# Optimization experiments

Measured on AMD Instinct MI355X. Metric: run time of the kernel, lower is better.

Reference implementation:

```python
import jax, jax.numpy as jnp
import numpy as np


def _mlp(x, w1, b1, w2, b2):
    # Linear->ReLU->Linear->ReLU (torch Linear: y = x @ W.T + b)
    return jax.nn.relu(jax.nn.relu(x @ w1.T + b1) @ w2.T + b2)


def _lstm_cell(x, h, c, wih, whh, bih, bhh):
    g = x @ wih.T + bih + h @ whh.T + bhh
    i, f, gg, o = jnp.split(g, 4, axis=-1)  # torch gate order i,f,g,o
    c = jax.nn.sigmoid(f) * c + jax.nn.sigmoid(i) * jnp.tanh(gg)
    h = jax.nn.sigmoid(o) * jnp.tanh(c)
    return h, c


def _decode(iml, img_features, mlp1_w1, mlp1_b1, mlp1_w2, mlp1_b2,
            mlp2_w1, mlp2_b1, mlp2_w2, mlp2_b2,
            lstm_wih, lstm_whh, lstm_bih, lstm_bhh,
            attn_w, attn_b, fc_w, fc_b, emb, max_seq_len):
    # iml: [B, H, K] flattened conv map; annotations are channel vectors per position
    ann = jnp.transpose(iml, (0, 2, 1))          # [B, K, H]
    mean_ann = jnp.mean(iml, axis=-1)            # [B, H]
    h0 = _mlp(mean_ann, mlp1_w1, mlp1_b1, mlp1_w2, mlp1_b2)
    c0 = _mlp(mean_ann, mlp2_w1, mlp2_b1, mlp2_w2, mlp2_b2)
    H = h0.shape[-1]
    # attn = Linear(2H, 1) on cat(ann, h): decompose into two dot products.
    w_a, w_h = attn_w[:H], attn_w[H:]
    e_ann = ann @ w_a + attn_b[0]                # [B, K], annotation part precomputed

    def step(carry, _):
        x, h, c = carry
        h, c = _lstm_cell(x, h, c, lstm_wih, lstm_whh, lstm_bih, lstm_bhh)
        e = e_ann + (h @ w_h)[:, None]           # [B, K] fused concat+linear scores
        alpha = jax.nn.softmax(e, axis=-1)       # [B, K]
        cs = jnp.einsum('bk,bkh->bh', alpha, ann)  # weighted context [B, H]
        logits = jnp.concatenate([h, cs], axis=-1) @ fc_w.T + fc_b  # [B, V]
        sample = jnp.argmax(logits, axis=-1)     # greedy token
        return (emb[sample], h, c), (logits, sample)

    _, (logits, samples) = jax.lax.scan(step, (img_features, h0, c0), None, length=max_seq_len)
    # scan stacks on axis 0 (time); move to [B, T, ...]
    return jnp.transpose(logits, (1, 0, 2)), jnp.transpose(samples, (1, 0))


def setup_inputs() -> dict:
    B, K, H, E, V, T = 64, 196, 512, 512, 10000, 30
    key = jax.random.key(0)
    ks = jax.random.split(key, 11)
    inv = 1.0 / np.sqrt(H)
    r = lambda i, shape, scale=1.0: jax.random.normal(ks[i], shape, jnp.float32) * scale
    return {
        'iml': r(0, (B, H, K)),
        'img_features': r(1, (B, E)),
        'mlp1_w1': r(2, (H, H), inv), 'mlp1_b1': jnp.zeros(H, jnp.float32),
        'mlp1_w2': r(3, (H, H), inv), 'mlp1_b2': jnp.zeros(H, jnp.float32),
        'mlp2_w1': r(4, (H, H), inv), 'mlp2_b1': jnp.zeros(H, jnp.float32),
        'mlp2_w2': r(5, (H, H), inv), 'mlp2_b2': jnp.zeros(H, jnp.float32),
        'lstm_wih': r(6, (4 * H, E), inv), 'lstm_whh': r(7, (4 * H, H), inv),
        'lstm_bih': jnp.zeros(4 * H, jnp.float32), 'lstm_bhh': jnp.zeros(4 * H, jnp.float32),
        'attn_w': r(8, (2 * H,), inv), 'attn_b': jnp.zeros(1, jnp.float32),
        'fc_w': r(9, (V, 2 * H), inv), 'fc_b': jnp.zeros(V, jnp.float32),
        'emb': r(10, (V, E)),
        'max_seq_len': T,
    }


def reference(iml, img_features, mlp1_w1, mlp1_b1, mlp1_w2, mlp1_b2,
              mlp2_w1, mlp2_b1, mlp2_w2, mlp2_b2,
              lstm_wih, lstm_whh, lstm_bih, lstm_bhh,
              attn_w, attn_b, fc_w, fc_b, emb, max_seq_len):
    all_logits, sampled_ids = _decode(
        iml, img_features, mlp1_w1, mlp1_b1, mlp1_w2, mlp1_b2,
        mlp2_w1, mlp2_b1, mlp2_w2, mlp2_b2,
        lstm_wih, lstm_whh, lstm_bih, lstm_bhh,
        attn_w, attn_b, fc_w, fc_b, emb, max_seq_len)
    return all_logits, sampled_ids
```

## Files before the change

### kernel.cpp

```cpp
#include <hip/hip_runtime.h>
#include <hip/hip_bf16.h>

#define B 64
#define KDIM 196
#define H 512
#define V 10000
#define TSTEPS 30
#define VP 10240
#define NVC 40
#define NSLOT 8
#define SLOTSTRIDE 16

typedef unsigned long long u64;
typedef unsigned int u32;

__device__ __forceinline__ u64 pack_vi(float v, int idx) {
    u32 kb = __float_as_uint(v);
    kb = (kb & 0x80000000u) ? ~kb : (kb | 0x80000000u);
    return ((u64)kb << 32) | (u32)(~(u32)idx);
}
__device__ __forceinline__ u32 best_idx_of_slots(const u64* __restrict__ slots, int b) {
    u64 best = slots[b * SLOTSTRIDE];
#pragma unroll
    for (int s = 1; s < NSLOT; ++s) { u64 v = slots[b * SLOTSTRIDE + s]; if (v > best) best = v; }
    return ~(u32)best;
}


__global__ void k_transpose_fc(const float* __restrict__ fcw, float* __restrict__ dst, int coloff) {
    __shared__ float tile[32][33];
    int v0 = blockIdx.x * 32, i0 = blockIdx.y * 32;
    int tx = threadIdx.x, ty = threadIdx.y;
#pragma unroll
    for (int r = 0; r < 32; r += 8) {
        int v = v0 + ty + r; int i = i0 + tx;
        tile[ty + r][tx] = (v < V) ? fcw[(size_t)v * 1024 + coloff + i] : 0.f;
    }
    __syncthreads();
#pragma unroll
    for (int r = 0; r < 32; r += 8) {
        int i = i0 + ty + r; int v = v0 + tx;
        dst[(size_t)i * VP + v] = tile[tx][ty + r];
    }
}

__global__ void k_build_wct(const float* __restrict__ wih, const float* __restrict__ whh,
                            float* __restrict__ dst) {
    __shared__ float tile[32][33];
    int j0 = blockIdx.x * 32, i0 = blockIdx.y * 32;
    int tx = threadIdx.x, ty = threadIdx.y;
#pragma unroll
    for (int r = 0; r < 32; r += 8) {
        int j = j0 + ty + r; int i = i0 + tx;
        tile[ty + r][tx] = (i < 512) ? wih[(size_t)j * 512 + i] : whh[(size_t)j * 512 + i - 512];
    }
    __syncthreads();
#pragma unroll
    for (int r = 0; r < 32; r += 8) {
        int i = i0 + ty + r; int j = j0 + tx;
        dst[(size_t)i * 2048 + j] = tile[tx][ty + r];
    }
}

__global__ void k_mean(const float* __restrict__ iml, float* __restrict__ mean) {
    int w = threadIdx.x >> 6, lane = threadIdx.x & 63;
    int row = blockIdx.x * 4 + w;
    const float* p = iml + (size_t)row * KDIM;
    float s = p[lane] + p[lane + 64] + p[lane + 128] + ((lane < 4) ? p[lane + 192] : 0.f);
#pragma unroll
    for (int off = 32; off; off >>= 1) s += __shfl_down(s, off);
    if (lane == 0) mean[row] = s * (1.f / 196.f);
}

__global__ void k_e_alpha(const float* __restrict__ iml, const float* __restrict__ attn_w,
                          float* __restrict__ alpha) {
    int b = blockIdx.x, t = threadIdx.x;
    __shared__ float wa[512];
    wa[t] = attn_w[t]; wa[t + 256] = attn_w[t + 256];
    __syncthreads();
    float acc = 0.f;
    if (t < KDIM) {
        const float* p = iml + (size_t)b * 512 * KDIM + t;
#pragma unroll 8
        for (int h = 0; h < 512; ++h) acc += p[(size_t)h * KDIM] * wa[h];
    }
    __shared__ float red[256];
    red[t] = (t < KDIM) ? acc : -__builtin_inff();
    __syncthreads();
    for (int s = 128; s; s >>= 1) { if (t < s) red[t] = fmaxf(red[t], red[t + s]); __syncthreads(); }
    float mx = red[0];
    __syncthreads();
    float ex = (t < KDIM) ? expf(acc - mx) : 0.f;
    red[t] = ex; __syncthreads();
    for (int s = 128; s; s >>= 1) { if (t < s) red[t] += red[t + s]; __syncthreads(); }
    if (t < KDIM) alpha[b * KDIM + t] = ex / red[0];
}

__global__ void k_cs(const float* __restrict__ iml, const float* __restrict__ alpha,
                     float* __restrict__ cs) {
    int w = threadIdx.x >> 6, lane = threadIdx.x & 63;
    int row = blockIdx.x * 4 + w;
    int b = row >> 9;
    const float* p = iml + (size_t)row * KDIM;
    const float* al = alpha + b * KDIM;
    float s = p[lane] * al[lane] + p[lane + 64] * al[lane + 64] + p[lane + 128] * al[lane + 128]
            + ((lane < 4) ? p[lane + 192] * al[lane + 192] : 0.f);
#pragma unroll
    for (int off = 32; off; off >>= 1) s += __shfl_down(s, off);
    if (lane == 0) cs[row] = s;
}

__global__ void k_dense_relu(const float* __restrict__ in, const float* __restrict__ W,
                             const float* __restrict__ bias, float* __restrict__ out, int ostride) {
    int b = blockIdx.y; int j = blockIdx.x * 256 + threadIdx.x;
    __shared__ float xs[512];
    xs[threadIdx.x] = in[b * 512 + threadIdx.x];
    xs[threadIdx.x + 256] = in[b * 512 + threadIdx.x + 256];
    __syncthreads();
    float acc = bias[j];
    const float4* w4 = (const float4*)(W + (size_t)j * 512);
#pragma unroll 4
    for (int i4 = 0; i4 < 128; ++i4) {
        float4 w = w4[i4];
        float4 x = *(const float4*)&xs[i4 * 4];
        acc += w.x * x.x + w.y * x.y + w.z * x.z + w.w * x.w;
    }
    out[(size_t)b * ostride + j] = fmaxf(acc, 0.f);
}

__global__ void k_gemm_big(const float* __restrict__ A, int astride,
                           const float* __restrict__ Wt, int wn,
                           float* __restrict__ part) {
    int jb = blockIdx.x, kc = blockIdx.y, bh = blockIdx.z;
    int w = threadIdx.x >> 6, lane = threadIdx.x & 63;
    int b0 = __builtin_amdgcn_readfirstlane(bh * 32 + w * 8);
    int k0 = kc * 64;
    int j0 = jb * 256 + lane * 4;
    float4 acc[8];
#pragma unroll
    for (int b = 0; b < 8; ++b) acc[b] = make_float4(0.f, 0.f, 0.f, 0.f);
    const float* wp = Wt + (size_t)k0 * wn + j0;
    const float* xp = A + (size_t)b0 * astride + k0;
#pragma unroll 8
    for (int kk = 0; kk < 64; ++kk) {
        float4 w4 = *(const float4*)(wp + (size_t)kk * wn);
#pragma unroll
        for (int b = 0; b < 8; ++b) {
            float xv = xp[(size_t)b * astride + kk];
            acc[b].x += xv * w4.x; acc[b].y += xv * w4.y;
            acc[b].z += xv * w4.z; acc[b].w += xv * w4.w;
        }
    }
#pragma unroll
    for (int b = 0; b < 8; ++b)
        *(float4*)(part + (size_t)(kc * 64 + b0 + b) * wn + j0) = acc[b];
}

__global__ void k_base_finish(const float* __restrict__ lpart, const float* __restrict__ fc_b,
                              float* __restrict__ base, u64* __restrict__ slots) {
    int b = blockIdx.y; int v = blockIdx.x * 256 + threadIdx.x;
    if (v < V) {
        float s = fc_b[v];
#pragma unroll
        for (int c = 0; c < 8; ++c) s += lpart[(size_t)(c * 64 + b) * VP + v];
        base[(size_t)b * VP + v] = s;
    }
    if (blockIdx.x == 0 && blockIdx.y == 0) {
#pragma unroll
        for (int i = 0; i < 4; ++i) slots[threadIdx.x + i * 256] = 0ull;
    }
}


__global__ void k_lstm_gemm(const float* __restrict__ img, const float* __restrict__ emb,
                            const u64* __restrict__ slots, const float* __restrict__ hbuf,
                            const float* __restrict__ WcT, float* __restrict__ part, int t0) {
    int jb = blockIdx.x, kc = blockIdx.y, bh = blockIdx.z;
    int w = threadIdx.x >> 6, lane = threadIdx.x & 63;
    int b0 = __builtin_amdgcn_readfirstlane(bh * 16 + w * 4);
    int k0 = kc * 64;
    int j0 = jb * 256 + lane * 4;
    const float* xr[4];
    if (k0 < 512) {
        if (t0) {
#pragma unroll
            for (int i = 0; i < 4; ++i) xr[i] = img + (size_t)(b0 + i) * 512 + k0;
        } else {
#pragma unroll
            for (int i = 0; i < 4; ++i) {
                u32 idx = best_idx_of_slots(slots, b0 + i);
                xr[i] = emb + (size_t)idx * 512 + k0;
            }
        }
    } else {
#pragma unroll
        for (int i = 0; i < 4; ++i) xr[i] = hbuf + (size_t)(b0 + i) * 512 + (k0 - 512);
    }
    float4 acc[4];
#pragma unroll
    for (int i = 0; i < 4; ++i) acc[i] = make_float4(0.f, 0.f, 0.f, 0.f);
    const float* wp = WcT + (size_t)k0 * 2048 + j0;
#pragma unroll 8
    for (int kk = 0; kk < 64; ++kk) {
        float4 w4 = *(const float4*)(wp + (size_t)kk * 2048);
#pragma unroll
        for (int i = 0; i < 4; ++i) {
            float xv = xr[i][kk];
            acc[i].x += xv * w4.x; acc[i].y += xv * w4.y;
            acc[i].z += xv * w4.z; acc[i].w += xv * w4.w;
        }
    }
#pragma unroll
    for (int i = 0; i < 4; ++i)
        *(float4*)(part + (size_t)(kc * 64 + b0 + i) * 2048 + j0) = acc[i];
}

__global__ void k_gates(const float* __restrict__ part, const float* __restrict__ bih,
                        const float* __restrict__ bhh, float* __restrict__ hbuf,
                        float* __restrict__ cbuf, u64* __restrict__ slots,
                        float* __restrict__ out1, int t) {
    int e = blockIdx.x * 256 + threadIdx.x;
    int b = e >> 9, jj = e & 511;
    float g[4];
#pragma unroll
    for (int gg = 0; gg < 4; ++gg) {
        int j = jj + gg * 512;
        float s = bih[j] + bhh[j];
#pragma unroll
        for (int c = 0; c < 16; ++c) s += part[(size_t)(c * 64 + b) * 2048 + j];
        g[gg] = s;
    }
    float ig = 1.f / (1.f + expf(-g[0]));
    float fg = 1.f / (1.f + expf(-g[1]));
    float gt = tanhf(g[2]);
    float og = 1.f / (1.f + expf(-g[3]));
    float c = fg * cbuf[e] + ig * gt;
    float h = og * tanhf(c);
    cbuf[e] = c; hbuf[e] = h;
    if (blockIdx.x == 0) {
        if (t > 0 && threadIdx.x < 64)
            out1[threadIdx.x * TSTEPS + (t - 1)] = (float)best_idx_of_slots(slots, threadIdx.x);
        __syncthreads();
#pragma unroll
        for (int i = 0; i < 4; ++i) slots[threadIdx.x + i * 256] = 0ull;
    }
}

__global__ void k_logits_gemm(const float* __restrict__ hbuf, const float* __restrict__ fcT,
                              float* __restrict__ part) {
    int jb = blockIdx.x, kc = blockIdx.y, bh = blockIdx.z;
    int w = threadIdx.x >> 6, lane = threadIdx.x & 63;
    int b0 = __builtin_amdgcn_readfirstlane(bh * 32 + w * 8);
    int k0 = kc * 128;
    int j0 = jb * 256 + lane * 4;
    float4 acc[8];
#pragma unroll
    for (int b = 0; b < 8; ++b) acc[b] = make_float4(0.f, 0.f, 0.f, 0.f);
    const float* wp = fcT + (size_t)k0 * VP + j0;
    const float* xp = hbuf + (size_t)b0 * 512 + k0;
#pragma unroll 8
    for (int kk = 0; kk < 128; ++kk) {
        float4 w4 = *(const float4*)(wp + (size_t)kk * VP);
#pragma unroll
        for (int b = 0; b < 8; ++b) {
            float xv = xp[(size_t)b * 512 + kk];
            acc[b].x += xv * w4.x; acc[b].y += xv * w4.y;
            acc[b].z += xv * w4.z; acc[b].w += xv * w4.w;
        }
    }
#pragma unroll
    for (int b = 0; b < 8; ++b)
        *(float4*)(part + (size_t)(kc * 64 + b0 + b) * VP + j0) = acc[b];
}

__global__ void k_logits_finish(const float* __restrict__ lpart, const float* __restrict__ base,
                                float* __restrict__ out0, u64* __restrict__ slots, int t) {
    int b = blockIdx.y, vc = blockIdx.x, tid = threadIdx.x;
    int lane = tid & 63;
    int v = vc * 256 + tid;
    float val = -__builtin_inff();
    if (v < V) {
        float s = base[(size_t)b * VP + v];
#pragma unroll
        for (int c = 0; c < 4; ++c) s += lpart[(size_t)(c * 64 + b) * VP + v];
        out0[((size_t)b * TSTEPS + t) * V + v] = s;
        val = s;
    }
    float m = val; int mi = (v < V) ? v : 0x7fffffff;
#pragma unroll
    for (int mk = 1; mk < 64; mk <<= 1) {
        float ov = __shfl_xor(m, mk);
        int oi = __shfl_xor(mi, mk);
        if (ov > m || (ov == m && oi < mi)) { m = ov; mi = oi; }
    }
    if (lane == 0) atomicMax(&slots[b * SLOTSTRIDE + (vc & 7)], pack_vi(m, mi));
}

__global__ void k_final_out1(const u64* __restrict__ slots, float* __restrict__ out1) {
    int b = threadIdx.x;
    if (b < B) out1[b * TSTEPS + (TSTEPS - 1)] = (float)best_idx_of_slots(slots, b);
}


extern "C" void kernel_launch(void* const* d_in, const int* in_sizes, int n_in,
                              void* d_out, int out_size, void* d_ws, size_t ws_size,
                              hipStream_t stream) {
    const float* iml   = (const float*)d_in[0];
    const float* img   = (const float*)d_in[1];
    const float* m1w1  = (const float*)d_in[2];
    const float* m1b1  = (const float*)d_in[3];
    const float* m1w2  = (const float*)d_in[4];
    const float* m1b2  = (const float*)d_in[5];
    const float* m2w1  = (const float*)d_in[6];
    const float* m2b1  = (const float*)d_in[7];
    const float* m2w2  = (const float*)d_in[8];
    const float* m2b2  = (const float*)d_in[9];
    const float* wih   = (const float*)d_in[10];
    const float* whh   = (const float*)d_in[11];
    const float* bih   = (const float*)d_in[12];
    const float* bhh   = (const float*)d_in[13];
    const float* attnw = (const float*)d_in[14];
    const float* fcw   = (const float*)d_in[16];
    const float* fcb   = (const float*)d_in[17];
    const float* emb   = (const float*)d_in[18];

    float* out0 = (float*)d_out;
    float* out1 = out0 + (size_t)B * TSTEPS * V;

    float* ws = (float*)d_ws;
    size_t off = 0;
    float* fcT   = ws + off; off += (size_t)512 * VP;
    float* WcT   = ws + off; off += (size_t)1024 * 2048;
    float* bigp  = ws + off; off += (size_t)8 * B * VP;
    float* gpart = ws + off; off += (size_t)16 * B * 2048;
    float* base  = ws + off; off += (size_t)B * VP;
    float* meanb = ws + off; off += B * 512;
    float* alpha = ws + off; off += B * KDIM;
    float* csb   = ws + off; off += B * 512;
    float* tmpb  = ws + off; off += B * 512;
    float* hbuf  = ws + off; off += B * 512;
    float* cbuf  = ws + off; off += B * 512;
    u64*   slots = (u64*)(ws + off); off += B * SLOTSTRIDE * 2;

    k_mean<<<dim3(8192), dim3(256), 0, stream>>>(iml, meanb);
    k_e_alpha<<<dim3(64), dim3(256), 0, stream>>>(iml, attnw, alpha);
    k_cs<<<dim3(8192), dim3(256), 0, stream>>>(iml, alpha, csb);
    k_dense_relu<<<dim3(2, 64), dim3(256), 0, stream>>>(meanb, m1w1, m1b1, tmpb, 512);
    k_dense_relu<<<dim3(2, 64), dim3(256), 0, stream>>>(tmpb, m1w2, m1b2, hbuf, 512);
    k_dense_relu<<<dim3(2, 64), dim3(256), 0, stream>>>(meanb, m2w1, m2b1, tmpb, 512);
    k_dense_relu<<<dim3(2, 64), dim3(256), 0, stream>>>(tmpb, m2w2, m2b2, cbuf, 512);

    k_transpose_fc<<<dim3(VP / 32, 16), dim3(32, 8), 0, stream>>>(fcw, fcT, 512);
    k_gemm_big<<<dim3(40, 8, 2), dim3(256), 0, stream>>>(csb, 512, fcT, VP, bigp);
    k_base_finish<<<dim3(NVC, 64), dim3(256), 0, stream>>>(bigp, fcb, base, slots);
    k_transpose_fc<<<dim3(VP / 32, 16), dim3(32, 8), 0, stream>>>(fcw, fcT, 0);
    k_build_wct<<<dim3(64, 32), dim3(32, 8), 0, stream>>>(wih, whh, WcT);

    for (int t = 0; t < TSTEPS; ++t) {
        k_lstm_gemm<<<dim3(8, 16, 4), dim3(256), 0, stream>>>(img, emb, slots, hbuf, WcT, gpart, (t == 0) ? 1 : 0);
        k_gates<<<dim3(128), dim3(256), 0, stream>>>(gpart, bih, bhh, hbuf, cbuf, slots, out1, t);
        k_logits_gemm<<<dim3(40, 4, 2), dim3(256), 0, stream>>>(hbuf, fcT, bigp);
        k_logits_finish<<<dim3(40, 64), dim3(256), 0, stream>>>(bigp, base, out0, slots, t);
    }
    k_final_out1<<<dim3(1), dim3(64), 0, stream>>>(slots, out1);
}
```

Measured before the change: 1.487 ms.

## Fuse prologue kernels, split attention scores, retile LSTM and logits GEMMs

Result: faster. 1.267 ms (-14.8%).

```diff
diff --git a/kernel.cpp b/kernel.cpp
--- a/kernel.cpp
+++ b/kernel.cpp
@@ -10,6 +10,7 @@
 #define NVC 40
 #define NSLOT 8
 #define SLOTSTRIDE 16
+#define NT 256
 
 typedef unsigned long long u64;
 typedef unsigned int u32;
@@ -23,7 +24,8 @@
     u64 best = slots[b * SLOTSTRIDE];
 #pragma unroll
     for (int s = 1; s < NSLOT; ++s) { u64 v = slots[b * SLOTSTRIDE + s]; if (v > best) best = v; }
-    return ~(u32)best;
+    u32 idx = ~(u32)best;
+    return idx < V ? idx : 0;
 }
 
 
@@ -62,27 +64,27 @@
     }
 }
 
-__global__ void k_mean(const float* __restrict__ iml, float* __restrict__ mean) {
-    int w = threadIdx.x >> 6, lane = threadIdx.x & 63;
-    int row = blockIdx.x * 4 + w;
-    const float* p = iml + (size_t)row * KDIM;
-    float s = p[lane] + p[lane + 64] + p[lane + 128] + ((lane < 4) ? p[lane + 192] : 0.f);
-#pragma unroll
-    for (int off = 32; off; off >>= 1) s += __shfl_down(s, off);
-    if (lane == 0) mean[row] = s * (1.f / 196.f);
-}
-
-__global__ void k_e_alpha(const float* __restrict__ iml, const float* __restrict__ attn_w,
-                          float* __restrict__ alpha) {
+__global__ void k_e_part(const float* __restrict__ iml, const float* __restrict__ attn_w,
+                         float* __restrict__ epart) {
+    int b = blockIdx.x, hc = blockIdx.y, t = threadIdx.x;
+    __shared__ float wa[64];
+    if (t < 64) wa[t] = attn_w[hc * 64 + t];
+    __syncthreads();
+    if (t < KDIM) {
+        const float* p = iml + (size_t)b * 512 * KDIM + (size_t)hc * 64 * KDIM + t;
+        float acc = 0.f;
+#pragma unroll 8
+        for (int h = 0; h < 64; ++h) acc += p[(size_t)h * KDIM] * wa[h];
+        epart[(size_t)(b * 8 + hc) * 208 + t] = acc;
+    }
+}
+
+__global__ void k_e_softmax(const float* __restrict__ epart, float* __restrict__ alpha) {
     int b = blockIdx.x, t = threadIdx.x;
-    __shared__ float wa[512];
-    wa[t] = attn_w[t]; wa[t + 256] = attn_w[t + 256];
-    __syncthreads();
     float acc = 0.f;
     if (t < KDIM) {
-        const float* p = iml + (size_t)b * 512 * KDIM + t;
-#pragma unroll 8
-        for (int h = 0; h < 512; ++h) acc += p[(size_t)h * KDIM] * wa[h];
+#pragma unroll
+        for (int c = 0; c < 8; ++c) acc += epart[(size_t)(b * 8 + c) * 208 + t];
     }
     __shared__ float red[256];
     red[t] = (t < KDIM) ? acc : -__builtin_inff();
@@ -96,22 +98,32 @@
     if (t < KDIM) alpha[b * KDIM + t] = ex / red[0];
 }
 
-__global__ void k_cs(const float* __restrict__ iml, const float* __restrict__ alpha,
-                     float* __restrict__ cs) {
+__global__ void k_mean_cs(const float* __restrict__ iml, const float* __restrict__ alpha,
+                          float* __restrict__ mean, float* __restrict__ cs) {
     int w = threadIdx.x >> 6, lane = threadIdx.x & 63;
     int row = blockIdx.x * 4 + w;
     int b = row >> 9;
     const float* p = iml + (size_t)row * KDIM;
     const float* al = alpha + b * KDIM;
-    float s = p[lane] * al[lane] + p[lane + 64] * al[lane + 64] + p[lane + 128] * al[lane + 128]
-            + ((lane < 4) ? p[lane + 192] * al[lane + 192] : 0.f);
-#pragma unroll
-    for (int off = 32; off; off >>= 1) s += __shfl_down(s, off);
-    if (lane == 0) cs[row] = s;
-}
-
-__global__ void k_dense_relu(const float* __restrict__ in, const float* __restrict__ W,
-                             const float* __restrict__ bias, float* __restrict__ out, int ostride) {
+    float p0 = p[lane], p1 = p[lane + 64], p2 = p[lane + 128];
+    float p3 = (lane < 4) ? p[lane + 192] : 0.f;
+    float a3 = (lane < 4) ? al[lane + 192] : 0.f;
+    float sm = p0 + p1 + p2 + p3;
+    float sc = p0 * al[lane] + p1 * al[lane + 64] + p2 * al[lane + 128] + p3 * a3;
+#pragma unroll
+    for (int off = 32; off; off >>= 1) { sm += __shfl_down(sm, off); sc += __shfl_down(sc, off); }
+    if (lane == 0) { mean[row] = sm * (1.f / 196.f); cs[row] = sc; }
+}
+
+__global__ void k_dense_relu2(const float* __restrict__ in0, const float* __restrict__ in1,
+                              const float* __restrict__ W0, const float* __restrict__ W1,
+                              const float* __restrict__ bi0, const float* __restrict__ bi1,
+                              float* __restrict__ o0, float* __restrict__ o1) {
+    int z = blockIdx.z;
+    const float* in = z ? in1 : in0;
+    const float* W  = z ? W1 : W0;
+    const float* bias = z ? bi1 : bi0;
+    float* out = z ? o1 : o0;
     int b = blockIdx.y; int j = blockIdx.x * 256 + threadIdx.x;
     __shared__ float xs[512];
     xs[threadIdx.x] = in[b * 512 + threadIdx.x];
@@ -125,7 +137,7 @@
         float4 x = *(const float4*)&xs[i4 * 4];
         acc += w.x * x.x + w.y * x.y + w.z * x.z + w.w * x.w;
     }
-    out[(size_t)b * ostride + j] = fmaxf(acc, 0.f);
+    out[(size_t)b * 512 + j] = fmaxf(acc, 0.f);
 }
 
 __global__ void k_gemm_big(const float* __restrict__ A, int astride,
@@ -177,41 +189,41 @@
                             const float* __restrict__ WcT, float* __restrict__ part, int t0) {
     int jb = blockIdx.x, kc = blockIdx.y, bh = blockIdx.z;
     int w = threadIdx.x >> 6, lane = threadIdx.x & 63;
-    int b0 = __builtin_amdgcn_readfirstlane(bh * 16 + w * 4);
+    int b0 = __builtin_amdgcn_readfirstlane(bh * 32 + w * 8);
     int k0 = kc * 64;
     int j0 = jb * 256 + lane * 4;
-    const float* xr[4];
+    const float* xp[8];
     if (k0 < 512) {
         if (t0) {
 #pragma unroll
-            for (int i = 0; i < 4; ++i) xr[i] = img + (size_t)(b0 + i) * 512 + k0;
+            for (int i = 0; i < 8; ++i) xp[i] = img + (size_t)(b0 + i) * 512 + k0;
         } else {
 #pragma unroll
-            for (int i = 0; i < 4; ++i) {
+            for (int i = 0; i < 8; ++i) {
                 u32 idx = best_idx_of_slots(slots, b0 + i);
-                xr[i] = emb + (size_t)idx * 512 + k0;
+                xp[i] = emb + (size_t)idx * 512 + k0;
             }
         }
     } else {
 #pragma unroll
-        for (int i = 0; i < 4; ++i) xr[i] = hbuf + (size_t)(b0 + i) * 512 + (k0 - 512);
-    }
-    float4 acc[4];
-#pragma unroll
-    for (int i = 0; i < 4; ++i) acc[i] = make_float4(0.f, 0.f, 0.f, 0.f);
+        for (int i = 0; i < 8; ++i) xp[i] = hbuf + (size_t)(b0 + i) * 512 + (k0 - 512);
+    }
+    float4 acc[8];
+#pragma unroll
+    for (int i = 0; i < 8; ++i) acc[i] = make_float4(0.f, 0.f, 0.f, 0.f);
     const float* wp = WcT + (size_t)k0 * 2048 + j0;
 #pragma unroll 8
     for (int kk = 0; kk < 64; ++kk) {
         float4 w4 = *(const float4*)(wp + (size_t)kk * 2048);
 #pragma unroll
-        for (int i = 0; i < 4; ++i) {
-            float xv = xr[i][kk];
+        for (int i = 0; i < 8; ++i) {
+            float xv = xp[i][kk];
             acc[i].x += xv * w4.x; acc[i].y += xv * w4.y;
             acc[i].z += xv * w4.z; acc[i].w += xv * w4.w;
         }
     }
 #pragma unroll
-    for (int i = 0; i < 4; ++i)
+    for (int i = 0; i < 8; ++i)
         *(float4*)(part + (size_t)(kc * 64 + b0 + i) * 2048 + j0) = acc[i];
 }
 
@@ -241,36 +253,8 @@
         if (t > 0 && threadIdx.x < 64)
             out1[threadIdx.x * TSTEPS + (t - 1)] = (float)best_idx_of_slots(slots, threadIdx.x);
         __syncthreads();
-#pragma unroll
-        for (int i = 0; i < 4; ++i) slots[threadIdx.x + i * 256] = 0ull;
-    }
-}
-
-__global__ void k_logits_gemm(const float* __restrict__ hbuf, const float* __restrict__ fcT,
-                              float* __restrict__ part) {
-    int jb = blockIdx.x, kc = blockIdx.y, bh = blockIdx.z;
-    int w = threadIdx.x >> 6, lane = threadIdx.x & 63;
-    int b0 = __builtin_amdgcn_readfirstlane(bh * 32 + w * 8);
-    int k0 = kc * 128;
-    int j0 = jb * 256 + lane * 4;
-    float4 acc[8];
-#pragma unroll
-    for (int b = 0; b < 8; ++b) acc[b] = make_float4(0.f, 0.f, 0.f, 0.f);
-    const float* wp = fcT + (size_t)k0 * VP + j0;
-    const float* xp = hbuf + (size_t)b0 * 512 + k0;
-#pragma unroll 8
-    for (int kk = 0; kk < 128; ++kk) {
-        float4 w4 = *(const float4*)(wp + (size_t)kk * VP);
-#pragma unroll
-        for (int b = 0; b < 8; ++b) {
-            float xv = xp[(size_t)b * 512 + kk];
-            acc[b].x += xv * w4.x; acc[b].y += xv * w4.y;
-            acc[b].z += xv * w4.z; acc[b].w += xv * w4.w;
-        }
-    }
-#pragma unroll
-    for (int b = 0; b < 8; ++b)
-        *(float4*)(part + (size_t)(kc * 64 + b0 + b) * VP + j0) = acc[b];
+        for (int i = threadIdx.x; i < B * SLOTSTRIDE; i += 256) slots[i] = 0ull;
+    }
 }
 
 __global__ void k_logits_finish(const float* __restrict__ lpart, const float* __restrict__ base,
@@ -282,7 +266,7 @@
     if (v < V) {
         float s = base[(size_t)b * VP + v];
 #pragma unroll
-        for (int c = 0; c < 4; ++c) s += lpart[(size_t)(c * 64 + b) * VP + v];
+        for (int c = 0; c < 8; ++c) s += lpart[(size_t)(c * 64 + b) * VP + v];
         out0[((size_t)b * TSTEPS + t) * V + v] = s;
         val = s;
     }
@@ -334,22 +318,21 @@
     float* bigp  = ws + off; off += (size_t)8 * B * VP;
     float* gpart = ws + off; off += (size_t)16 * B * 2048;
     float* base  = ws + off; off += (size_t)B * VP;
+    float* epart = ws + off; off += (size_t)B * 8 * 208;
     float* meanb = ws + off; off += B * 512;
     float* alpha = ws + off; off += B * KDIM;
     float* csb   = ws + off; off += B * 512;
-    float* tmpb  = ws + off; off += B * 512;
+    float* tmp1  = ws + off; off += B * 512;
+    float* tmp2  = ws + off; off += B * 512;
     float* hbuf  = ws + off; off += B * 512;
     float* cbuf  = ws + off; off += B * 512;
     u64*   slots = (u64*)(ws + off); off += B * SLOTSTRIDE * 2;
 
-    k_mean<<<dim3(8192), dim3(256), 0, stream>>>(iml, meanb);
-    k_e_alpha<<<dim3(64), dim3(256), 0, stream>>>(iml, attnw, alpha);
-    k_cs<<<dim3(8192), dim3(256), 0, stream>>>(iml, alpha, csb);
-    k_dense_relu<<<dim3(2, 64), dim3(256), 0, stream>>>(meanb, m1w1, m1b1, tmpb, 512);
-    k_dense_relu<<<dim3(2, 64), dim3(256), 0, stream>>>(tmpb, m1w2, m1b2, hbuf, 512);
-    k_dense_relu<<<dim3(2, 64), dim3(256), 0, stream>>>(meanb, m2w1, m2b1, tmpb, 512);
-    k_dense_relu<<<dim3(2, 64), dim3(256), 0, stream>>>(tmpb, m2w2, m2b2, cbuf, 512);
-
+    k_e_part<<<dim3(64, 8), dim3(256), 0, stream>>>(iml, attnw, epart);
+    k_e_softmax<<<dim3(64), dim3(256), 0, stream>>>(epart, alpha);
+    k_mean_cs<<<dim3(8192), dim3(256), 0, stream>>>(iml, alpha, meanb, csb);
+    k_dense_relu2<<<dim3(2, 64, 2), dim3(256), 0, stream>>>(meanb, meanb, m1w1, m2w1, m1b1, m2b1, tmp1, tmp2);
+    k_dense_relu2<<<dim3(2, 64, 2), dim3(256), 0, stream>>>(tmp1, tmp2, m1w2, m2w2, m1b2, m2b2, hbuf, cbuf);
     k_transpose_fc<<<dim3(VP / 32, 16), dim3(32, 8), 0, stream>>>(fcw, fcT, 512);
     k_gemm_big<<<dim3(40, 8, 2), dim3(256), 0, stream>>>(csb, 512, fcT, VP, bigp);
     k_base_finish<<<dim3(NVC, 64), dim3(256), 0, stream>>>(bigp, fcb, base, slots);
@@ -357,10 +340,10 @@
     k_build_wct<<<dim3(64, 32), dim3(32, 8), 0, stream>>>(wih, whh, WcT);
 
     for (int t = 0; t < TSTEPS; ++t) {
-        k_lstm_gemm<<<dim3(8, 16, 4), dim3(256), 0, stream>>>(img, emb, slots, hbuf, WcT, gpart, (t == 0) ? 1 : 0);
+        k_lstm_gemm<<<dim3(8, 16, 2), dim3(256), 0, stream>>>(img, emb, slots, hbuf, WcT, gpart, (t == 0) ? 1 : 0);
         k_gates<<<dim3(128), dim3(256), 0, stream>>>(gpart, bih, bhh, hbuf, cbuf, slots, out1, t);
-        k_logits_gemm<<<dim3(40, 4, 2), dim3(256), 0, stream>>>(hbuf, fcT, bigp);
-        k_logits_finish<<<dim3(40, 64), dim3(256), 0, stream>>>(bigp, base, out0, slots, t);
+        k_gemm_big<<<dim3(40, 8, 2), dim3(256), 0, stream>>>(hbuf, 512, fcT, VP, bigp);
+        k_logits_finish<<<dim3(NVC, 64), dim3(256), 0, stream>>>(bigp, base, out0, slots, t);
     }
     k_final_out1<<<dim3(1), dim3(64), 0, stream>>>(slots, out1);
 }
```
